# Kernel tuning notes

Measured on AMD Instinct MI355X. Metric: run time of the kernel, lower is better.

The kernel has to match this reference:

```python
import jax, jax.numpy as jnp
import numpy as np

NODE_DIM = 64
HIDDEN_DIM = 128
N_GRAPHS = 8
NODES_PER_GRAPH = 2048
N_TOTAL = N_GRAPHS * NODES_PER_GRAPH
N_EDGES = N_TOTAL * 32


def setup_inputs() -> dict:
    key = jax.random.key(0)
    ks = jax.random.split(key, 8)
    x = jax.random.normal(ks[0], (N_TOTAL, NODE_DIM), dtype=jnp.float32)
    edge_index = jax.random.randint(ks[1], (2, N_EDGES), 0, N_TOTAL, dtype=jnp.int64)
    # NNConv root weights + biases (glorot-ish scale)
    W1 = jax.random.normal(ks[2], (NODE_DIM, HIDDEN_DIM), dtype=jnp.float32) / np.sqrt(NODE_DIM)
    b1 = jnp.zeros((HIDDEN_DIM,), dtype=jnp.float32)
    W2 = jax.random.normal(ks[3], (HIDDEN_DIM, HIDDEN_DIM), dtype=jnp.float32) / np.sqrt(HIDDEN_DIM)
    b2 = jnp.zeros((HIDDEN_DIM,), dtype=jnp.float32)
    # link-predictor Linear(2*hidden -> 1)
    w_lin = jax.random.normal(ks[4], (2 * HIDDEN_DIM,), dtype=jnp.float32) / np.sqrt(2 * HIDDEN_DIM)
    b_lin = jnp.zeros((), dtype=jnp.float32)
    return {
        "x": x, "edge_index": edge_index,
        "W1": W1, "b1": b1, "W2": W2, "b2": b2,
        "w_lin": w_lin, "b_lin": b_lin,
        "n_graphs": N_GRAPHS, "nodes_per_graph": NODES_PER_GRAPH,
    }


def _nnconv_ones(x, src, dst, W_root, bias, n_total):
    # callable_my returns ones(in*out) -> per-edge weight matrix is all-ones [in,out],
    # so message_e = x[src_e] @ ones = sum(x[src_e]) broadcast over out channels.
    s = x.sum(axis=-1)                         # [N]
    msg = jnp.take(s, src, axis=0)             # [E]
    agg = jax.ops.segment_sum(msg, dst, num_segments=n_total)           # [N]
    deg = jax.ops.segment_sum(jnp.ones_like(msg), dst, num_segments=n_total)
    agg = agg / jnp.where(deg > 0, deg, 1.0)   # mean aggregation; 0 for isolated nodes
    return agg[:, None] + x @ W_root + bias    # [N, out]


def reference(x, edge_index, W1, b1, W2, b2, w_lin, b_lin, n_graphs, nodes_per_graph):
    n_total = n_graphs * nodes_per_graph
    src, dst = edge_index[0], edge_index[1]
    # dropout layers are identity in eval mode
    h = jax.nn.relu(_nnconv_ones(x, src, dst, W1, b1, n_total))
    h = jax.nn.relu(_nnconv_ones(h, src, dst, W2, b2, n_total))
    # all-pairs concat + Linear(2H->1) + sigmoid, per graph, vectorized:
    # score[b,i,j] = sigmoid(h[b,i].w_left + h[b,j].w_right + b)
    H = h.shape[-1]
    hb = h.reshape(n_graphs, nodes_per_graph, H)
    left = hb @ w_lin[:H]                      # [B, N]
    right = hb @ w_lin[H:]                     # [B, N]
    scores = jax.nn.sigmoid(left[:, :, None] + right[:, None, :] + b_lin)
    # original returns a tuple of per-graph flat [N*N] tensors; equal sizes -> [B, N*N]
    return scores.reshape(n_graphs, nodes_per_graph * nodes_per_graph)
```

## Files before the change

kernel.cpp:

```cpp
#include <hip/hip_runtime.h>

#define N_TOTAL 16384
#define NODE_DIM 64
#define HIDDEN 128
#define NPG 2048
#define NGRAPH 8
#define NPART 128

typedef float v4f __attribute__((ext_vector_type(4)));

#define C1      (1 << 19)
#define SC1     8192.0f
#define ISC1    (1.0f / 8192.0f)
#define SC2     16384.0f
#define ISC2    (1.0f / 16384.0f)

__device__ __forceinline__ int detect_flag(const int* ei_words) {
    int lane = threadIdx.x & 63;
    int nz = 0;
    for (int i = lane; i < 256; i += 64)
        if (ei_words[2 * i + 1] != 0) nz = 1;
    return __any(nz) ? 1 : 0;
}

__global__ __launch_bounds__(256) void kS1(
    const float* __restrict__ x, float* __restrict__ s1) {
    int tid = threadIdx.x;
    int r   = blockIdx.x * 16 + (tid >> 4);
    int q   = tid & 15;
    float4 v = ((const float4*)x)[r * 16 + q];
    float sum = v.x + v.y + v.z + v.w;
    sum += __shfl_xor(sum, 1);
    sum += __shfl_xor(sum, 2);
    sum += __shfl_xor(sum, 4);
    sum += __shfl_xor(sum, 8);
    if (q == 0) s1[r] = sum;
}

__global__ __launch_bounds__(512) void kScat1(
    const void* __restrict__ ei_raw, int E, const float* __restrict__ s1,
    unsigned* __restrict__ pcomb) {
    __shared__ unsigned acc[N_TOTAL];
    int tid = threadIdx.x, b = blockIdx.x;
    int f = detect_flag((const int*)ei_raw);
    for (int i = tid; i < N_TOTAL; i += 512) acc[i] = 0u;
    __syncthreads();
    int epb = (E + NPART - 1) / NPART;
    int e0 = b * epb, e1 = min(E, e0 + epb);
    if (f) {
        const int* ep = (const int*)ei_raw;
        for (int e = e0 + tid; e < e1; e += 512) {
            int src = ep[e], dst = ep[E + e];
            int q = (int)lrintf(s1[src] * SC1);
            atomicAdd(&acc[dst], (1u << 26) + (unsigned)(q + C1));
        }
    } else {
        const long long* ep = (const long long*)ei_raw;
        for (int e = e0 + tid; e < e1; e += 512) {
            int src = (int)ep[e], dst = (int)ep[E + e];
            int q = (int)lrintf(s1[src] * SC1);
            atomicAdd(&acc[dst], (1u << 26) + (unsigned)(q + C1));
        }
    }
    __syncthreads();
    unsigned* outp = pcomb + (size_t)b * N_TOTAL;
    for (int i = tid; i < N_TOTAL; i += 512) outp[i] = acc[i];
}

__global__ __launch_bounds__(512) void kScat2(
    const void* __restrict__ ei_raw, int E, const float* __restrict__ s2,
    int* __restrict__ ps2) {
    __shared__ int acc[N_TOTAL];
    int tid = threadIdx.x, b = blockIdx.x;
    int f = detect_flag((const int*)ei_raw);
    for (int i = tid; i < N_TOTAL; i += 512) acc[i] = 0;
    __syncthreads();
    int epb = (E + NPART - 1) / NPART;
    int e0 = b * epb, e1 = min(E, e0 + epb);
    if (f) {
        const int* ep = (const int*)ei_raw;
        for (int e = e0 + tid; e < e1; e += 512) {
            int src = ep[e], dst = ep[E + e];
            int q = (int)lrintf(s2[src] * SC2);
            atomicAdd((unsigned*)&acc[dst], (unsigned)q);
        }
    } else {
        const long long* ep = (const long long*)ei_raw;
        for (int e = e0 + tid; e < e1; e += 512) {
            int src = (int)ep[e], dst = (int)ep[E + e];
            int q = (int)lrintf(s2[src] * SC2);
            atomicAdd((unsigned*)&acc[dst], (unsigned)q);
        }
    }
    __syncthreads();
    int* outp = ps2 + (size_t)b * N_TOTAL;
    for (int i = tid; i < N_TOTAL; i += 512) outp[i] = acc[i];
}

__global__ __launch_bounds__(256) void k3_layer1(
    const float* __restrict__ x, const float* __restrict__ W1,
    const float* __restrict__ b1, const unsigned* __restrict__ pcomb,
    float* __restrict__ h1, float* __restrict__ s2, float* __restrict__ degf) {
    __shared__ float W1s[NODE_DIM * HIDDEN];
    __shared__ float xs[16 * NODE_DIM];
    __shared__ float mean1s[16];
    int tid  = threadIdx.x;
    int base = blockIdx.x * 16;
    {
        int r = tid >> 4, j = tid & 15;
        int grow = base + r;
        int c = 0, sq = 0;
        #pragma unroll
        for (int k = 0; k < 8; ++k) {
            unsigned v = pcomb[(size_t)(j + 16 * k) * N_TOTAL + grow];
            int n_i = (int)(v >> 26);
            c  += n_i;
            sq += (int)(v & 0x03FFFFFFu) - n_i * C1;
        }
        for (int off = 8; off; off >>= 1) {
            c  += __shfl_xor(c, off);
            sq += __shfl_xor(sq, off);
        }
        if (j == 0) {
            mean1s[r] = c > 0 ? ((float)sq * ISC1) / (float)c : 0.f;
            degf[grow] = (float)c;
        }
    }
    {
        const float4* Wv = (const float4*)W1;
        float4* Wsv = (float4*)W1s;
        for (int i = tid; i < NODE_DIM * HIDDEN / 4; i += 256) Wsv[i] = Wv[i];
        const float4* xv = (const float4*)(x + base * NODE_DIM);
        float4* xsv = (float4*)xs;
        for (int i = tid; i < 16 * NODE_DIM / 4; i += 256) xsv[i] = xv[i];
    }
    __syncthreads();
    int lane32 = tid & 31;
    int rg     = tid >> 5;
    int c4     = lane32 * 4;
    int row0   = rg * 2, row1 = rg * 2 + 1;
    float a00 = 0.f, a01 = 0.f, a02 = 0.f, a03 = 0.f;
    float a10 = 0.f, a11 = 0.f, a12 = 0.f, a13 = 0.f;
    #pragma unroll
    for (int k = 0; k < NODE_DIM; ++k) {
        float4 w = *(const float4*)&W1s[k * HIDDEN + c4];
        float x0 = xs[row0 * NODE_DIM + k];
        float x1 = xs[row1 * NODE_DIM + k];
        a00 = fmaf(x0, w.x, a00); a01 = fmaf(x0, w.y, a01);
        a02 = fmaf(x0, w.z, a02); a03 = fmaf(x0, w.w, a03);
        a10 = fmaf(x1, w.x, a10); a11 = fmaf(x1, w.y, a11);
        a12 = fmaf(x1, w.z, a12); a13 = fmaf(x1, w.w, a13);
    }
    float4 bb = *(const float4*)&b1[c4];
    #pragma unroll
    for (int rr = 0; rr < 2; ++rr) {
        int row  = rr ? row1 : row0;
        int grow = base + row;
        float aa0 = rr ? a10 : a00, aa1 = rr ? a11 : a01;
        float aa2 = rr ? a12 : a02, aa3 = rr ? a13 : a03;
        float mean = mean1s[row];
        float4 v;
        v.x = fmaxf(mean + aa0 + bb.x, 0.f);
        v.y = fmaxf(mean + aa1 + bb.y, 0.f);
        v.z = fmaxf(mean + aa2 + bb.z, 0.f);
        v.w = fmaxf(mean + aa3 + bb.w, 0.f);
        *(float4*)&h1[grow * HIDDEN + c4] = v;
        float rs = v.x + v.y + v.z + v.w;
        for (int off = 16; off; off >>= 1) rs += __shfl_xor(rs, off);
        if (lane32 == 0) s2[grow] = rs;
    }
}

__global__ __launch_bounds__(256) void k6_layer2(
    const float* __restrict__ h1, const float* __restrict__ W2,
    const float* __restrict__ b2, const int* __restrict__ ps2,
    const float* __restrict__ degf, const float* __restrict__ wlin,
    float* __restrict__ left, float* __restrict__ right) {
    __shared__ float W2s[64 * HIDDEN];
    __shared__ float hs[16 * HIDDEN];
    __shared__ float mean2s[16];
    int tid  = threadIdx.x;
    int base = blockIdx.x * 16;
    {
        int r = tid >> 4, j = tid & 15;
        int grow = base + r;
        int sq = 0;
        #pragma unroll
        for (int k = 0; k < 8; ++k)
            sq += ps2[(size_t)(j + 16 * k) * N_TOTAL + grow];
        for (int off = 8; off; off >>= 1) sq += __shfl_xor(sq, off);
        if (j == 0) {
            float d = degf[grow];
            mean2s[r] = d > 0.f ? ((float)sq * ISC2) / d : 0.f;
        }
    }
    {
        const float4* hv = (const float4*)(h1 + base * HIDDEN);
        float4* hsv = (float4*)hs;
        for (int i = tid; i < 16 * HIDDEN / 4; i += 256) hsv[i] = hv[i];
    }
    int lane32 = tid & 31;
    int rg     = tid >> 5;
    int c4     = lane32 * 4;
    int row0   = rg * 2, row1 = rg * 2 + 1;
    float a00 = 0.f, a01 = 0.f, a02 = 0.f, a03 = 0.f;
    float a10 = 0.f, a11 = 0.f, a12 = 0.f, a13 = 0.f;
    for (int chunk = 0; chunk < 2; ++chunk) {
        __syncthreads();
        {
            const float4* Wv = (const float4*)(W2 + chunk * 64 * HIDDEN);
            float4* Wsv = (float4*)W2s;
            for (int i = tid; i < 64 * HIDDEN / 4; i += 256) Wsv[i] = Wv[i];
        }
        __syncthreads();
        int kb = chunk * 64;
        #pragma unroll 8
        for (int k = 0; k < 64; ++k) {
            float4 w = *(const float4*)&W2s[k * HIDDEN + c4];
            float h0 = hs[row0 * HIDDEN + kb + k];
            float h1v = hs[row1 * HIDDEN + kb + k];
            a00 = fmaf(h0, w.x, a00);  a01 = fmaf(h0, w.y, a01);
            a02 = fmaf(h0, w.z, a02);  a03 = fmaf(h0, w.w, a03);
            a10 = fmaf(h1v, w.x, a10); a11 = fmaf(h1v, w.y, a11);
            a12 = fmaf(h1v, w.z, a12); a13 = fmaf(h1v, w.w, a13);
        }
    }
    float4 bb  = *(const float4*)&b2[c4];
    float4 wl  = *(const float4*)&wlin[c4];
    float4 wr  = *(const float4*)&wlin[HIDDEN + c4];
    #pragma unroll
    for (int rr = 0; rr < 2; ++rr) {
        int row  = rr ? row1 : row0;
        int grow = base + row;
        float aa0 = rr ? a10 : a00, aa1 = rr ? a11 : a01;
        float aa2 = rr ? a12 : a02, aa3 = rr ? a13 : a03;
        float ag = mean2s[row];
        float h0e = fmaxf(ag + aa0 + bb.x, 0.f);
        float h1e = fmaxf(ag + aa1 + bb.y, 0.f);
        float h2e = fmaxf(ag + aa2 + bb.z, 0.f);
        float h3e = fmaxf(ag + aa3 + bb.w, 0.f);
        float lp = h0e * wl.x + h1e * wl.y + h2e * wl.z + h3e * wl.w;
        float rp = h0e * wr.x + h1e * wr.y + h2e * wr.z + h3e * wr.w;
        for (int off = 16; off; off >>= 1) {
            lp += __shfl_xor(lp, off);
            rp += __shfl_xor(rp, off);
        }
        if (lane32 == 0) { left[grow] = lp; right[grow] = rp; }
    }
}

__global__ __launch_bounds__(256) void k7_scores(
    const float* __restrict__ left, const float* __restrict__ right,
    const float* __restrict__ blin, float* __restrict__ out) {
    int tid  = threadIdx.x;
    int base = blockIdx.x * 16;
    float bl = blin[0];
    const v4f* rv4 = (const v4f*)(right + ((base >> 11) << 11));
    #pragma unroll 4
    for (int rr = 0; rr < 16; ++rr) {
        int r = base + rr;
        float L = left[r] + bl;
        v4f* orow = (v4f*)out + ((size_t)r << 9);
        #pragma unroll
        for (int c = tid; c < 512; c += 256) {
            v4f rv = rv4[c];
            v4f o;
            o.x = 1.f / (1.f + __expf(-(L + rv.x)));
            o.y = 1.f / (1.f + __expf(-(L + rv.y)));
            o.z = 1.f / (1.f + __expf(-(L + rv.z)));
            o.w = 1.f / (1.f + __expf(-(L + rv.w)));
            __builtin_nontemporal_store(o, orow + c);
        }
    }
}

extern "C" void kernel_launch(void* const* d_in, const int* in_sizes, int n_in,
                              void* d_out, int out_size, void* d_ws, size_t ws_size,
                              hipStream_t stream) {
    const float* x    = (const float*)d_in[0];
    const void*  ei   = d_in[1];
    const float* W1   = (const float*)d_in[2];
    const float* b1   = (const float*)d_in[3];
    const float* W2   = (const float*)d_in[4];
    const float* b2   = (const float*)d_in[5];
    const float* wlin = (const float*)d_in[6];
    const float* blin = (const float*)d_in[7];
    int E = in_sizes[1] / 2;

    float* ws    = (float*)d_ws;
    float* s1    = ws;
    float* s2    = ws + 1 * N_TOTAL;
    float* degf  = ws + 2 * N_TOTAL;
    float* left  = ws + 3 * N_TOTAL;
    float* right = ws + 4 * N_TOTAL;
    float* h1    = ws + 5 * N_TOTAL;
    float* out   = (float*)d_out;

    unsigned* pcomb = (unsigned*)d_out;
    int*      ps2   = (int*)d_out + (size_t)NPART * N_TOTAL;

    kS1<<<N_TOTAL / 16, 256, 0, stream>>>(x, s1);
    kScat1<<<NPART, 512, 0, stream>>>(ei, E, s1, pcomb);
    k3_layer1<<<N_TOTAL / 16, 256, 0, stream>>>(x, W1, b1, pcomb, h1, s2, degf);
    kScat2<<<NPART, 512, 0, stream>>>(ei, E, s2, ps2);
    k6_layer2<<<N_TOTAL / 16, 256, 0, stream>>>(h1, W2, b2, ps2, degf, wlin, left, right);
    k7_scores<<<N_TOTAL / 16, 256, 0, stream>>>(left, right, blin, out);
}
```

Measured before the change: 99.23 us.

## Pack edge indices once, halve scatter partitions, widen GEMM row tiles

The first scatter pass now writes each edge as one 32-bit word (16-bit src and dst), so the second scatter pass reads that compact array instead of the raw int64 edge index. This cuts the edge-index traffic in the second pass. The number of scatter partitions drops from 128 to 64, which halves the size of the partial-sum arrays the layer kernels must reduce, though with fewer blocks in each scatter kernel. The layer kernels now process 32 rows per block with a 4x4 register tile per thread and write h1 with nontemporal stores. This reuses each weight load across more rows at the cost of more registers. The 16-bit packing only works because the node count is below 65536.

```diff
diff --git a/kernel.cpp b/kernel.cpp
--- a/kernel.cpp
+++ b/kernel.cpp
@@ -5,7 +5,7 @@
 #define HIDDEN 128
 #define NPG 2048
 #define NGRAPH 8
-#define NPART 128
+#define NPART 64
 
 typedef float v4f __attribute__((ext_vector_type(4)));
 
@@ -39,7 +39,7 @@
 
 __global__ __launch_bounds__(512) void kScat1(
     const void* __restrict__ ei_raw, int E, const float* __restrict__ s1,
-    unsigned* __restrict__ pcomb) {
+    unsigned* __restrict__ pcomb, unsigned* __restrict__ dec) {
     __shared__ unsigned acc[N_TOTAL];
     int tid = threadIdx.x, b = blockIdx.x;
     int f = detect_flag((const int*)ei_raw);
@@ -51,6 +51,7 @@
         const int* ep = (const int*)ei_raw;
         for (int e = e0 + tid; e < e1; e += 512) {
             int src = ep[e], dst = ep[E + e];
+            dec[e] = (unsigned)src | ((unsigned)dst << 16);
             int q = (int)lrintf(s1[src] * SC1);
             atomicAdd(&acc[dst], (1u << 26) + (unsigned)(q + C1));
         }
@@ -58,6 +59,7 @@
         const long long* ep = (const long long*)ei_raw;
         for (int e = e0 + tid; e < e1; e += 512) {
             int src = (int)ep[e], dst = (int)ep[E + e];
+            dec[e] = (unsigned)src | ((unsigned)dst << 16);
             int q = (int)lrintf(s1[src] * SC1);
             atomicAdd(&acc[dst], (1u << 26) + (unsigned)(q + C1));
         }
@@ -68,29 +70,19 @@
 }
 
 __global__ __launch_bounds__(512) void kScat2(
-    const void* __restrict__ ei_raw, int E, const float* __restrict__ s2,
+    const unsigned* __restrict__ dec, int E, const float* __restrict__ s2,
     int* __restrict__ ps2) {
     __shared__ int acc[N_TOTAL];
     int tid = threadIdx.x, b = blockIdx.x;
-    int f = detect_flag((const int*)ei_raw);
     for (int i = tid; i < N_TOTAL; i += 512) acc[i] = 0;
     __syncthreads();
     int epb = (E + NPART - 1) / NPART;
     int e0 = b * epb, e1 = min(E, e0 + epb);
-    if (f) {
-        const int* ep = (const int*)ei_raw;
-        for (int e = e0 + tid; e < e1; e += 512) {
-            int src = ep[e], dst = ep[E + e];
-            int q = (int)lrintf(s2[src] * SC2);
-            atomicAdd((unsigned*)&acc[dst], (unsigned)q);
-        }
-    } else {
-        const long long* ep = (const long long*)ei_raw;
-        for (int e = e0 + tid; e < e1; e += 512) {
-            int src = (int)ep[e], dst = (int)ep[E + e];
-            int q = (int)lrintf(s2[src] * SC2);
-            atomicAdd((unsigned*)&acc[dst], (unsigned)q);
-        }
+    for (int e = e0 + tid; e < e1; e += 512) {
+        unsigned d32 = dec[e];
+        int src = (int)(d32 & 0xFFFFu), dst = (int)(d32 >> 16);
+        int q = (int)lrintf(s2[src] * SC2);
+        atomicAdd((unsigned*)&acc[dst], (unsigned)q);
     }
     __syncthreads();
     int* outp = ps2 + (size_t)b * N_TOTAL;
@@ -102,22 +94,22 @@
     const float* __restrict__ b1, const unsigned* __restrict__ pcomb,
     float* __restrict__ h1, float* __restrict__ s2, float* __restrict__ degf) {
     __shared__ float W1s[NODE_DIM * HIDDEN];
-    __shared__ float xs[16 * NODE_DIM];
-    __shared__ float mean1s[16];
+    __shared__ float xs[32 * NODE_DIM];
+    __shared__ float mean1s[32];
     int tid  = threadIdx.x;
-    int base = blockIdx.x * 16;
+    int base = blockIdx.x * 32;
     {
-        int r = tid >> 4, j = tid & 15;
+        int r = tid >> 3, j = tid & 7;
         int grow = base + r;
         int c = 0, sq = 0;
         #pragma unroll
         for (int k = 0; k < 8; ++k) {
-            unsigned v = pcomb[(size_t)(j + 16 * k) * N_TOTAL + grow];
+            unsigned v = pcomb[(size_t)(j + 8 * k) * N_TOTAL + grow];
             int n_i = (int)(v >> 26);
             c  += n_i;
             sq += (int)(v & 0x03FFFFFFu) - n_i * C1;
         }
-        for (int off = 8; off; off >>= 1) {
+        for (int off = 4; off; off >>= 1) {
             c  += __shfl_xor(c, off);
             sq += __shfl_xor(sq, off);
         }
@@ -132,39 +124,42 @@
         for (int i = tid; i < NODE_DIM * HIDDEN / 4; i += 256) Wsv[i] = Wv[i];
         const float4* xv = (const float4*)(x + base * NODE_DIM);
         float4* xsv = (float4*)xs;
-        for (int i = tid; i < 16 * NODE_DIM / 4; i += 256) xsv[i] = xv[i];
+        for (int i = tid; i < 32 * NODE_DIM / 4; i += 256) xsv[i] = xv[i];
     }
     __syncthreads();
     int lane32 = tid & 31;
     int rg     = tid >> 5;
     int c4     = lane32 * 4;
-    int row0   = rg * 2, row1 = rg * 2 + 1;
-    float a00 = 0.f, a01 = 0.f, a02 = 0.f, a03 = 0.f;
-    float a10 = 0.f, a11 = 0.f, a12 = 0.f, a13 = 0.f;
+    int r0     = rg * 4;
+    float a[4][4];
+    #pragma unroll
+    for (int i = 0; i < 4; ++i)
+        #pragma unroll
+        for (int jj = 0; jj < 4; ++jj) a[i][jj] = 0.f;
     #pragma unroll
     for (int k = 0; k < NODE_DIM; ++k) {
         float4 w = *(const float4*)&W1s[k * HIDDEN + c4];
-        float x0 = xs[row0 * NODE_DIM + k];
-        float x1 = xs[row1 * NODE_DIM + k];
-        a00 = fmaf(x0, w.x, a00); a01 = fmaf(x0, w.y, a01);
-        a02 = fmaf(x0, w.z, a02); a03 = fmaf(x0, w.w, a03);
-        a10 = fmaf(x1, w.x, a10); a11 = fmaf(x1, w.y, a11);
-        a12 = fmaf(x1, w.z, a12); a13 = fmaf(x1, w.w, a13);
+        #pragma unroll
+        for (int i = 0; i < 4; ++i) {
+            float xv = xs[(r0 + i) * NODE_DIM + k];
+            a[i][0] = fmaf(xv, w.x, a[i][0]);
+            a[i][1] = fmaf(xv, w.y, a[i][1]);
+            a[i][2] = fmaf(xv, w.z, a[i][2]);
+            a[i][3] = fmaf(xv, w.w, a[i][3]);
+        }
     }
     float4 bb = *(const float4*)&b1[c4];
     #pragma unroll
-    for (int rr = 0; rr < 2; ++rr) {
-        int row  = rr ? row1 : row0;
+    for (int i = 0; i < 4; ++i) {
+        int row  = r0 + i;
         int grow = base + row;
-        float aa0 = rr ? a10 : a00, aa1 = rr ? a11 : a01;
-        float aa2 = rr ? a12 : a02, aa3 = rr ? a13 : a03;
         float mean = mean1s[row];
-        float4 v;
-        v.x = fmaxf(mean + aa0 + bb.x, 0.f);
-        v.y = fmaxf(mean + aa1 + bb.y, 0.f);
-        v.z = fmaxf(mean + aa2 + bb.z, 0.f);
-        v.w = fmaxf(mean + aa3 + bb.w, 0.f);
-        *(float4*)&h1[grow * HIDDEN + c4] = v;
+        v4f v;
+        v.x = fmaxf(mean + a[i][0] + bb.x, 0.f);
+        v.y = fmaxf(mean + a[i][1] + bb.y, 0.f);
+        v.z = fmaxf(mean + a[i][2] + bb.z, 0.f);
+        v.w = fmaxf(mean + a[i][3] + bb.w, 0.f);
+        __builtin_nontemporal_store(v, (v4f*)&h1[grow * HIDDEN + c4]);
         float rs = v.x + v.y + v.z + v.w;
         for (int off = 16; off; off >>= 1) rs += __shfl_xor(rs, off);
         if (lane32 == 0) s2[grow] = rs;
@@ -177,18 +172,18 @@
     const float* __restrict__ degf, const float* __restrict__ wlin,
     float* __restrict__ left, float* __restrict__ right) {
     __shared__ float W2s[64 * HIDDEN];
-    __shared__ float hs[16 * HIDDEN];
-    __shared__ float mean2s[16];
+    __shared__ float hs[32 * HIDDEN];
+    __shared__ float mean2s[32];
     int tid  = threadIdx.x;
-    int base = blockIdx.x * 16;
+    int base = blockIdx.x * 32;
     {
-        int r = tid >> 4, j = tid & 15;
+        int r = tid >> 3, j = tid & 7;
         int grow = base + r;
         int sq = 0;
         #pragma unroll
         for (int k = 0; k < 8; ++k)
-            sq += ps2[(size_t)(j + 16 * k) * N_TOTAL + grow];
-        for (int off = 8; off; off >>= 1) sq += __shfl_xor(sq, off);
+            sq += ps2[(size_t)(j + 8 * k) * N_TOTAL + grow];
+        for (int off = 4; off; off >>= 1) sq += __shfl_xor(sq, off);
         if (j == 0) {
             float d = degf[grow];
             mean2s[r] = d > 0.f ? ((float)sq * ISC2) / d : 0.f;
@@ -197,14 +192,17 @@
     {
         const float4* hv = (const float4*)(h1 + base * HIDDEN);
         float4* hsv = (float4*)hs;
-        for (int i = tid; i < 16 * HIDDEN / 4; i += 256) hsv[i] = hv[i];
+        for (int i = tid; i < 32 * HIDDEN / 4; i += 256) hsv[i] = hv[i];
     }
     int lane32 = tid & 31;
     int rg     = tid >> 5;
     int c4     = lane32 * 4;
-    int row0   = rg * 2, row1 = rg * 2 + 1;
-    float a00 = 0.f, a01 = 0.f, a02 = 0.f, a03 = 0.f;
-    float a10 = 0.f, a11 = 0.f, a12 = 0.f, a13 = 0.f;
+    int r0     = rg * 4;
+    float a[4][4];
+    #pragma unroll
+    for (int i = 0; i < 4; ++i)
+        #pragma unroll
+        for (int jj = 0; jj < 4; ++jj) a[i][jj] = 0.f;
     for (int chunk = 0; chunk < 2; ++chunk) {
         __syncthreads();
         {
@@ -217,28 +215,28 @@
         #pragma unroll 8
         for (int k = 0; k < 64; ++k) {
             float4 w = *(const float4*)&W2s[k * HIDDEN + c4];
-            float h0 = hs[row0 * HIDDEN + kb + k];
-            float h1v = hs[row1 * HIDDEN + kb + k];
-            a00 = fmaf(h0, w.x, a00);  a01 = fmaf(h0, w.y, a01);
-            a02 = fmaf(h0, w.z, a02);  a03 = fmaf(h0, w.w, a03);
-            a10 = fmaf(h1v, w.x, a10); a11 = fmaf(h1v, w.y, a11);
-            a12 = fmaf(h1v, w.z, a12); a13 = fmaf(h1v, w.w, a13);
+            #pragma unroll
+            for (int i = 0; i < 4; ++i) {
+                float hv = hs[(r0 + i) * HIDDEN + kb + k];
+                a[i][0] = fmaf(hv, w.x, a[i][0]);
+                a[i][1] = fmaf(hv, w.y, a[i][1]);
+                a[i][2] = fmaf(hv, w.z, a[i][2]);
+                a[i][3] = fmaf(hv, w.w, a[i][3]);
+            }
         }
     }
     float4 bb  = *(const float4*)&b2[c4];
     float4 wl  = *(const float4*)&wlin[c4];
     float4 wr  = *(const float4*)&wlin[HIDDEN + c4];
     #pragma unroll
-    for (int rr = 0; rr < 2; ++rr) {
-        int row  = rr ? row1 : row0;
+    for (int i = 0; i < 4; ++i) {
+        int row  = r0 + i;
         int grow = base + row;
-        float aa0 = rr ? a10 : a00, aa1 = rr ? a11 : a01;
-        float aa2 = rr ? a12 : a02, aa3 = rr ? a13 : a03;
         float ag = mean2s[row];
-        float h0e = fmaxf(ag + aa0 + bb.x, 0.f);
-        float h1e = fmaxf(ag + aa1 + bb.y, 0.f);
-        float h2e = fmaxf(ag + aa2 + bb.z, 0.f);
-        float h3e = fmaxf(ag + aa3 + bb.w, 0.f);
+        float h0e = fmaxf(ag + a[i][0] + bb.x, 0.f);
+        float h1e = fmaxf(ag + a[i][1] + bb.y, 0.f);
+        float h2e = fmaxf(ag + a[i][2] + bb.z, 0.f);
+        float h3e = fmaxf(ag + a[i][3] + bb.w, 0.f);
         float lp = h0e * wl.x + h1e * wl.y + h2e * wl.z + h3e * wl.w;
         float rp = h0e * wr.x + h1e * wr.y + h2e * wr.z + h3e * wr.w;
         for (int off = 16; off; off >>= 1) {
@@ -294,15 +292,16 @@
     float* left  = ws + 3 * N_TOTAL;
     float* right = ws + 4 * N_TOTAL;
     float* h1    = ws + 5 * N_TOTAL;
+    unsigned* dec = (unsigned*)(h1 + (size_t)HIDDEN * N_TOTAL);
     float* out   = (float*)d_out;
 
     unsigned* pcomb = (unsigned*)d_out;
     int*      ps2   = (int*)d_out + (size_t)NPART * N_TOTAL;
 
     kS1<<<N_TOTAL / 16, 256, 0, stream>>>(x, s1);
-    kScat1<<<NPART, 512, 0, stream>>>(ei, E, s1, pcomb);
-    k3_layer1<<<N_TOTAL / 16, 256, 0, stream>>>(x, W1, b1, pcomb, h1, s2, degf);
-    kScat2<<<NPART, 512, 0, stream>>>(ei, E, s2, ps2);
-    k6_layer2<<<N_TOTAL / 16, 256, 0, stream>>>(h1, W2, b2, ps2, degf, wlin, left, right);
+    kScat1<<<NPART, 512, 0, stream>>>(ei, E, s1, pcomb, dec);
+    k3_layer1<<<N_TOTAL / 32, 256, 0, stream>>>(x, W1, b1, pcomb, h1, s2, degf);
+    kScat2<<<NPART, 512, 0, stream>>>(dec, E, s2, ps2);
+    k6_layer2<<<N_TOTAL / 32, 256, 0, stream>>>(h1, W2, b2, ps2, degf, wlin, left, right);
     k7_scores<<<N_TOTAL / 16, 256, 0, stream>>>(left, right, blin, out);
 }
```

Result: faster. 90.19 us (-9.1%).
